# Performance work log

Measured on AMD Instinct MI355X. Metric: run time of the kernel, lower is better.

Reference implementation:

```python
import jax, jax.numpy as jnp
import numpy as np

B_SZ, SEQ = 2, 4096
D_MODEL = 1024
EXPAND = 2
HEADDIM = 64
D_STATE = 128
D_CONV = 4
INTER = EXPAND * D_MODEL            # 2048
NHEADS = INTER // HEADDIM           # 32
CONV_DIM = INTER + 2 * D_STATE      # n_groups = 1
PROJ_DIM = 2 * INTER + 2 * D_STATE + NHEADS
CHUNK = 256
EPS = 1e-5


def setup_inputs() -> dict:
    key = jax.random.key(0)
    k = jax.random.split(key, 6)
    u = jax.random.normal(k[0], (B_SZ, SEQ, D_MODEL), jnp.float32)
    in_proj_w = jax.random.normal(k[1], (D_MODEL, PROJ_DIM), jnp.float32) * 0.02
    conv_w = jax.random.normal(k[2], (CONV_DIM, D_CONV), jnp.float32) * 0.2
    conv_b = jnp.zeros((CONV_DIM,), jnp.float32)
    # dt init in [1e-3, 1e-1], inverse-softplus so softplus(dt_bias) recovers dt
    dt0 = jnp.exp(jax.random.uniform(k[3], (NHEADS,), jnp.float32, np.log(1e-3), np.log(1e-1)))
    dt_bias = jnp.log(jnp.expm1(dt0))
    A_log = jnp.log(jnp.arange(1, NHEADS + 1, dtype=jnp.float32))
    D_param = jnp.ones((NHEADS,), jnp.float32)
    norm_w = jnp.ones((INTER,), jnp.float32)
    out_proj_w = jax.random.normal(k[4], (INTER, D_MODEL), jnp.float32) * 0.02
    return {"u": u, "in_proj_w": in_proj_w, "conv_w": conv_w, "conv_b": conv_b,
            "dt_bias": dt_bias, "A_log": A_log, "D_param": D_param,
            "norm_w": norm_w, "out_proj_w": out_proj_w}


def _silu(x):
    return x * jax.nn.sigmoid(x)


def _causal_conv1d(x, w, b):
    # depthwise causal conv; x (b,s,c), w (c,k); tap k-1 is the current timestep
    k = w.shape[1]
    xp = jnp.pad(x, ((0, 0), (k - 1, 0), (0, 0)))
    y = b
    for i in range(k):
        y = y + xp[:, i:i + x.shape[1], :] * w[:, i]
    return y


def _segsum(x):
    # x (..., l) -> (..., l, l); segsum[i, j] = sum_{j < k <= i} x[k], -inf above diag
    l = x.shape[-1]
    cs = jnp.cumsum(x, -1)
    d = cs[..., :, None] - cs[..., None, :]
    mask = jnp.tril(jnp.ones((l, l), dtype=bool))
    return jnp.where(mask, d, -jnp.inf)


def _ssd(x, dt, A, Bm, Cm):
    # Mamba-2 chunked SSD (ssd_minimal_discrete with X = x*dt, Adt = A*dt).
    # x (b,s,h,p), dt (b,s,h), A (h,), Bm/Cm (b,s,n)
    b, s, h, p = x.shape
    n = Bm.shape[-1]
    c = s // CHUNK
    X = (x * dt[..., None]).reshape(b, c, CHUNK, h, p)          # (b,c,l,h,p)
    Adt = (dt * A).reshape(b, c, CHUNK, h).transpose(0, 3, 1, 2)  # (b,h,c,l)
    Bc = Bm.reshape(b, c, CHUNK, n)
    Cc = Cm.reshape(b, c, CHUNK, n)
    A_cum = jnp.cumsum(Adt, -1)                                  # (b,h,c,l)
    L = jnp.exp(_segsum(Adt))                                    # (b,h,c,l,l) causal decay
    # intra-chunk (diagonal blocks)
    scores = jnp.einsum('bcln,bcsn->bcls', Cc, Bc)               # (b,c,l,l)
    Y_diag = jnp.einsum('bhcls,bcshp->bclhp', scores[:, None] * L, X)
    # per-chunk final states
    decay_states = jnp.exp(A_cum[..., -1:] - A_cum)              # (b,h,c,l)
    states = jnp.einsum('bcln,bhcl,bclhp->bchpn', Bc, decay_states, X)
    # inter-chunk recurrence on chunk states
    A_chunk = jnp.pad(A_cum[..., -1], ((0, 0), (0, 0), (1, 0)))  # (b,h,c+1)
    decay_chunk = jnp.exp(_segsum(A_chunk))                      # (b,h,c+1,c+1)
    states = jnp.concatenate([jnp.zeros_like(states[:, :1]), states], axis=1)  # (b,c+1,h,p,n)
    states = jnp.einsum('bhzc,bchpn->bzhpn', decay_chunk, states)[:, :-1]      # (b,c,h,p,n)
    # state -> output contribution
    Y_off = jnp.einsum('bcln,bchpn,bhcl->bclhp', Cc, states, jnp.exp(A_cum))
    return (Y_diag + Y_off).reshape(b, s, h, p)


def reference(u, in_proj_w, conv_w, conv_b, dt_bias, A_log, D_param, norm_w, out_proj_w):
    b, s, _ = u.shape
    zxbcdt = u @ in_proj_w                                       # (b,s,PROJ_DIM)
    z = zxbcdt[..., :INTER]
    xBC = zxbcdt[..., INTER:INTER + CONV_DIM]
    dt = zxbcdt[..., INTER + CONV_DIM:]
    xBC = _silu(_causal_conv1d(xBC, conv_w, conv_b))
    x = xBC[..., :INTER]
    Bm = xBC[..., INTER:INTER + D_STATE]
    Cm = xBC[..., INTER + D_STATE:]
    dt = jax.nn.softplus(dt + dt_bias)                           # (b,s,h)
    A = -jnp.exp(A_log)                                          # (h,)
    xh = x.reshape(b, s, NHEADS, HEADDIM)
    y = _ssd(xh, dt, A, Bm, Cm) + D_param[None, None, :, None] * xh
    y = y.reshape(b, s, INTER)
    g = y * _silu(z)                                             # gated RMSNorm
    g = g * jax.lax.rsqrt(jnp.mean(g * g, -1, keepdims=True) + EPS) * norm_w
    return g @ out_proj_w
```

## Files before the change

kernel.cpp:

```cpp
#include <hip/hip_runtime.h>
#include <hip/hip_bf16.h>

#define B_SZ 2
#define SEQ 4096
#define DMODEL 1024
#define INTER 2048
#define NHEADS 32
#define HDIM 64
#define DSTATE 128
#define DCONV 4
#define CONVDIM 2304
#define PROJDIM 4384
#define CHUNK 256
#define NCHUNK 16
#define ROWS (B_SZ*SEQ)
#define NGEMM 4352
#define NMAIN 4096

typedef __hip_bfloat16 bf16;
typedef short bfx8 __attribute__((ext_vector_type(8)));
typedef float f32x4 __attribute__((ext_vector_type(4)));

__device__ __forceinline__ float sigmoidf_(float x){ return 1.f/(1.f+expf(-x)); }
__device__ __forceinline__ float b2f(bf16 v){ return __bfloat162float(v); }
__device__ __forceinline__ bf16 f2b(float v){ return __float2bfloat16(v); }
__device__ __forceinline__ float bits2f(unsigned short u){ return __uint_as_float(((unsigned)u) << 16); }
__device__ __forceinline__ unsigned short f2bits(float v){ bf16 t = __float2bfloat16(v); return *(unsigned short*)&t; }

#define MFMA16(a,b,c) __builtin_amdgcn_mfma_f32_16x16x32_bf16(a,b,c,0,0,0)

__global__ void zero_out_kernel(float* o, int n){
  int i = blockIdx.x*256 + threadIdx.x;
  if (i < n) o[i] = 0.f;
}

__global__ __launch_bounds__(256) void transcast_kernel(const float* __restrict__ in,
    bf16* __restrict__ outT, int R, int ld, int coff){
  __shared__ float t[64][65];
  int r0 = blockIdx.y*64, c0 = blockIdx.x*64;
  int tid = threadIdx.x;
  #pragma unroll
  for (int i = 0; i < 16; i++){
    int idx = tid + i*256;
    int r = idx >> 6, c = idx & 63;
    t[r][c] = in[(size_t)(r0+r)*ld + coff + c0 + c];
  }
  __syncthreads();
  #pragma unroll
  for (int i = 0; i < 16; i++){
    int idx = tid + i*256;
    int c = idx >> 6, r = idx & 63;
    outT[(size_t)(c0+c)*R + r0 + r] = f2b(t[r][c]);
  }
}

__device__ __forceinline__ void stage8(const bf16* __restrict__ g, int Kdim,
    int tile0, int k0, char* region, int h, int tid){
  #pragma unroll
  for (int l = 0; l < 2; l++){
    int o  = h*16384 + (l*512 + tid)*16;
    int os = o ^ (((o >> 7) & 7) << 4);
    const bf16* src = g + (size_t)(tile0 + (os >> 7))*Kdim + k0 + ((os & 127) >> 1);
    __builtin_amdgcn_global_load_lds(
      (const __attribute__((address_space(1))) void*)src,
      (__attribute__((address_space(3))) void*)(region + h*16384 + (l*512 + (tid >> 6)*64)*16),
      16, 0, 0);
  }
}
__device__ __forceinline__ bfx8 fr8(const char* region, int row, int colbyte){
  int o = row*128 + colbyte;
  o ^= ((row & 7) << 4);
  return *(const bfx8*)(region + o);
}

#define LGKM0  asm volatile("s_waitcnt lgkmcnt(0)" ::: "memory"); __builtin_amdgcn_sched_barrier(0)
#define VM4    asm volatile("s_waitcnt vmcnt(4)" ::: "memory")
#define VM0    asm volatile("s_waitcnt vmcnt(0)" ::: "memory")
#define BAR    __builtin_amdgcn_s_barrier()
#define PRIO1  __builtin_amdgcn_s_setprio(1)
#define PRIO0  __builtin_amdgcn_s_setprio(0)

#define MFMA_QUAD(MH, NH, BARR)                                                \
  PRIO1;                                                                       \
  _Pragma("unroll") for (int m = 0; m < 4; m++)                                \
    _Pragma("unroll") for (int n = 0; n < 2; n++)                              \
      _Pragma("unroll") for (int kk = 0; kk < 2; kk++)                         \
        acc[(MH)+m][(NH)+n] = MFMA16(aF[m][kk], BARR[n][kk], acc[(MH)+m][(NH)+n]); \
  PRIO0

#define GEMM8_BODY(K_, NBX_)                                                   \
  extern __shared__ char lds[];                                                \
  char* A0 = lds;          char* B0 = lds + 32768;                             \
  char* A1 = lds + 65536;  char* B1 = lds + 98304;                             \
  const int tid = threadIdx.x, lane = tid & 63, wid = tid >> 6;                \
  const int wm = wid >> 2, wn = wid & 3;                                       \
  int nb = (blockIdx.x & 7)*((int)gridDim.x >> 3) + (blockIdx.x >> 3);         \
  const int bx = nb % (NBX_), by = nb / (NBX_);                                \
  const int row0 = by*256, col0 = bx*256;                                      \
  f32x4 acc[8][4] = {};                                                        \
  bfx8 aF[4][2], b01[2][2], b23[2][2];                                         \
  const int frow = lane & 15;                                                  \
  const int fcb0 = (lane >> 4)*16;                                             \
  const int JLAST = (K_)/128 - 1;                                              \
  stage8(Bt, K_, col0, 0,  B0, 0, tid);                                        \
  stage8(Bt, K_, col0, 0,  B0, 1, tid);                                        \
  stage8(A,  K_, row0, 0,  A0, 0, tid);                                        \
  stage8(A,  K_, row0, 0,  A0, 1, tid);                                        \
  stage8(Bt, K_, col0, 64, B1, 0, tid);                                        \
  stage8(Bt, K_, col0, 64, B1, 1, tid);                                        \
  VM4;                                                                         \
  BAR;                                                                         \
  _Pragma("unroll 1")                                                          \
  for (int j = 0; j <= JLAST; j++){                                            \
    const int kO  = j*128 + 64;                                                \
    const int kS1 = (j*128 + 128) & ((K_) - 1);                                \
    const int kS2 = (j*128 + 192) & ((K_) - 1);                                \
    stage8(A, K_, row0, kO, A1, 0, tid);                                       \
    _Pragma("unroll") for (int m = 0; m < 4; m++)                              \
      _Pragma("unroll") for (int kk = 0; kk < 2; kk++)                         \
        aF[m][kk] = fr8(A0, wm*128 + m*16 + frow, kk*64 + fcb0);               \
    _Pragma("unroll") for (int n = 0; n < 2; n++)                              \
      _Pragma("unroll") for (int kk = 0; kk < 2; kk++)                         \
        b01[n][kk] = fr8(B0, wn*64 + n*16 + frow, kk*64 + fcb0);               \
    LGKM0;                                                                     \
    MFMA_QUAD(0, 0, b01);                                                      \
    BAR;                                                                       \
    stage8(A, K_, row0, kO, A1, 1, tid);                                       \
    _Pragma("unroll") for (int n = 0; n < 2; n++)                              \
      _Pragma("unroll") for (int kk = 0; kk < 2; kk++)                         \
        b23[n][kk] = fr8(B0, wn*64 + (n+2)*16 + frow, kk*64 + fcb0);           \
    LGKM0;                                                                     \
    MFMA_QUAD(0, 2, b23);                                                      \
    BAR;                                                                       \
    if (j < JLAST) stage8(Bt, K_, col0, kS1, B0, 0, tid);                      \
    _Pragma("unroll") for (int m = 0; m < 4; m++)                              \
      _Pragma("unroll") for (int kk = 0; kk < 2; kk++)                         \
        aF[m][kk] = fr8(A0, wm*128 + (m+4)*16 + frow, kk*64 + fcb0);           \
    LGKM0;                                                                     \
    MFMA_QUAD(4, 0, b01);                                                      \
    BAR;                                                                       \
    if (j < JLAST){ stage8(Bt, K_, col0, kS1, B0, 1, tid); VM4; }              \
    else { VM0; }                                                              \
    MFMA_QUAD(4, 2, b23);                                                      \
    BAR;                                                                       \
    if (j < JLAST) stage8(A, K_, row0, kS1, A0, 0, tid);                       \
    _Pragma("unroll") for (int m = 0; m < 4; m++)                              \
      _Pragma("unroll") for (int kk = 0; kk < 2; kk++)                         \
        aF[m][kk] = fr8(A1, wm*128 + m*16 + frow, kk*64 + fcb0);               \
    _Pragma("unroll") for (int n = 0; n < 2; n++)                              \
      _Pragma("unroll") for (int kk = 0; kk < 2; kk++)                         \
        b01[n][kk] = fr8(B1, wn*64 + n*16 + frow, kk*64 + fcb0);               \
    LGKM0;                                                                     \
    MFMA_QUAD(0, 0, b01);                                                      \
    BAR;                                                                       \
    if (j < JLAST) stage8(A, K_, row0, kS1, A0, 1, tid);                       \
    _Pragma("unroll") for (int n = 0; n < 2; n++)                              \
      _Pragma("unroll") for (int kk = 0; kk < 2; kk++)                         \
        b23[n][kk] = fr8(B1, wn*64 + (n+2)*16 + frow, kk*64 + fcb0);           \
    LGKM0;                                                                     \
    MFMA_QUAD(0, 2, b23);                                                      \
    BAR;                                                                       \
    if (j < JLAST) stage8(Bt, K_, col0, kS2, B1, 0, tid);                      \
    _Pragma("unroll") for (int m = 0; m < 4; m++)                              \
      _Pragma("unroll") for (int kk = 0; kk < 2; kk++)                         \
        aF[m][kk] = fr8(A1, wm*128 + (m+4)*16 + frow, kk*64 + fcb0);           \
    LGKM0;                                                                     \
    MFMA_QUAD(4, 0, b01);                                                      \
    BAR;                                                                       \
    if (j < JLAST) stage8(Bt, K_, col0, kS2, B1, 1, tid);                      \
    VM4;                                                                       \
    MFMA_QUAD(4, 2, b23);                                                      \
    BAR;                                                                       \
  }

#define SST_STRIDE 280

__global__ __launch_bounds__(512, 2) void gemm8_inproj(const bf16* __restrict__ A,
    const bf16* __restrict__ Bt, bf16* __restrict__ z, bf16* __restrict__ xbc){
  GEMM8_BODY(DMODEL, 16)
  unsigned short* sst = (unsigned short*)lds;
  #pragma unroll 1
  for (int half = 0; half < 2; half++){
    if (wm == half){
      #pragma unroll
      for (int m = 0; m < 8; m++)
        #pragma unroll
        for (int n = 0; n < 4; n++)
          #pragma unroll
          for (int r = 0; r < 4; r++){
            int rl = m*16 + (lane>>4)*4 + r;
            sst[rl*SST_STRIDE + wn*64 + n*16 + (lane&15)] = f2bits(acc[m][n][r]);
          }
    }
    BAR;
    #pragma unroll
    for (int i = 0; i < 8; i++){
      int q = tid + i*512;
      int rl = q >> 5, c8 = (q & 31)*8;
      bfx8 v = *(const bfx8*)(sst + rl*SST_STRIDE + c8);
      int gr = row0 + half*128 + rl, gc = col0 + c8;
      if (gc < INTER) *(bfx8*)(z + (size_t)gr*INTER + gc) = v;
      else            *(bfx8*)(xbc + (size_t)gr*CONVDIM + (gc - INTER)) = v;
    }
    BAR;
  }
}

#define MFMA_GEMM_BODY(K_, EPILOGUE)                                           \
  __shared__ unsigned short As[128*64];                                        \
  __shared__ unsigned short Bs[128*64];                                        \
  const int tid = threadIdx.x;                                                 \
  const int lane = tid & 63, wid = tid >> 6;                                   \
  const int wm = wid >> 1, wn = wid & 1;                                       \
  const int row0 = blockIdx.y*128, col0 = blockIdx.x*128;                      \
  f32x4 acc[4][4] = {};                                                        \
  const int rstg = wid*32 + ((lane>>3)&7);                                     \
  const int kstg = (lane&7)*8;                                                 \
  for (int k0 = 0; k0 < (K_); k0 += 64){                                       \
    _Pragma("unroll")                                                          \
    for (int j = 0; j < 4; j++){                                               \
      const bf16* gA = A + (size_t)(row0 + rstg + j*8)*(K_) + k0 + kstg;       \
      __builtin_amdgcn_global_load_lds(                                        \
        (const __attribute__((address_space(1))) void*)gA,                     \
        (__attribute__((address_space(3))) void*)(As + (wid*32 + j*8)*64),     \
        16, 0, 0);                                                             \
      const bf16* gB = Bt + (size_t)(col0 + rstg + j*8)*(K_) + k0 + kstg;      \
      __builtin_amdgcn_global_load_lds(                                        \
        (const __attribute__((address_space(1))) void*)gB,                     \
        (__attribute__((address_space(3))) void*)(Bs + (wid*32 + j*8)*64),     \
        16, 0, 0);                                                             \
    }                                                                          \
    __syncthreads();                                                           \
    _Pragma("unroll")                                                          \
    for (int kk = 0; kk < 2; kk++){                                            \
      bfx8 af[4], bfr[4];                                                      \
      _Pragma("unroll")                                                        \
      for (int m = 0; m < 4; m++)                                              \
        af[m] = *(const bfx8*)(As + (wm*64 + m*16 + (lane&15))*64              \
                               + kk*32 + (lane>>4)*8);                         \
      _Pragma("unroll")                                                        \
      for (int n = 0; n < 4; n++)                                              \
        bfr[n] = *(const bfx8*)(Bs + (wn*64 + n*16 + (lane&15))*64             \
                                + kk*32 + (lane>>4)*8);                        \
      _Pragma("unroll")                                                        \
      for (int m = 0; m < 4; m++)                                              \
        _Pragma("unroll")                                                      \
        for (int n = 0; n < 4; n++)                                            \
          acc[m][n] = MFMA16(af[m], bfr[n], acc[m][n]);                        \
    }                                                                          \
    __syncthreads();                                                           \
  }                                                                            \
  _Pragma("unroll")                                                            \
  for (int m = 0; m < 4; m++){                                                 \
    int row = row0 + wm*64 + m*16 + (lane>>4)*4;                               \
    _Pragma("unroll")                                                          \
    for (int n = 0; n < 4; n++){                                               \
      int col = col0 + wn*64 + n*16 + (lane&15);                               \
      _Pragma("unroll")                                                        \
      for (int r = 0; r < 4; r++){                                             \
        float v = acc[m][n][r];                                                \
        int rr = row + r;                                                      \
        EPILOGUE                                                               \
      }                                                                        \
    }                                                                          \
  }

__global__ __launch_bounds__(256) void gemm_mfma_inproj(const bf16* __restrict__ A,
    const bf16* __restrict__ Bt, bf16* __restrict__ z, bf16* __restrict__ xbc){
  MFMA_GEMM_BODY(DMODEL,
    if (col < INTER) z[(size_t)rr*INTER + col] = f2b(v);
    else             xbc[(size_t)rr*CONVDIM + (col - INTER)] = f2b(v);
  )
}
__global__ __launch_bounds__(256) void gemm_mfma_strip(const bf16* __restrict__ A,
    const bf16* __restrict__ Bt, bf16* __restrict__ xbc){
  MFMA_GEMM_BODY(DMODEL,
    xbc[(size_t)rr*CONVDIM + 2048 + col] = f2b(v);
  )
}
__global__ __launch_bounds__(256) void gemm_mfma_outproj(const bf16* __restrict__ A,
    const bf16* __restrict__ Bt, float* __restrict__ C){
  MFMA_GEMM_BODY(INTER,
    C[(size_t)rr*DMODEL + col] = v;
  )
}

__global__ __launch_bounds__(256) void dt_partial(const float* __restrict__ u,
    const float* __restrict__ w_in, float* __restrict__ partial,
    unsigned short* __restrict__ u_bf){
  __shared__ float wsm[128][33];
  __shared__ float us[64][133];
  int ks = blockIdx.x, row0 = blockIdx.y*64;
  int k0 = ks*128;
  int tid = threadIdx.x;
  #pragma unroll
  for (int i = 0; i < 16; i++){
    int idx = tid + i*256;
    int r = idx >> 5, c = idx & 31;
    wsm[r][c] = w_in[(size_t)(k0 + r)*PROJDIM + NGEMM + c];
  }
  #pragma unroll
  for (int i = 0; i < 8; i++){
    int idx = tid + i*256;
    int r = idx >> 5, c4 = idx & 31;
    float4 v = *(const float4*)(u + (size_t)(row0 + r)*DMODEL + k0 + c4*4);
    us[r][c4*4+0] = v.x; us[r][c4*4+1] = v.y; us[r][c4*4+2] = v.z; us[r][c4*4+3] = v.w;
    ushort4 w;
    w.x = f2bits(v.x); w.y = f2bits(v.y); w.z = f2bits(v.z); w.w = f2bits(v.w);
    *(ushort4*)(u_bf + (size_t)(row0 + r)*DMODEL + k0 + c4*4) = w;
  }
  __syncthreads();
  int col = tid & 31, r0 = tid >> 5;
  float acc[8] = {};
  #pragma unroll 4
  for (int kk4 = 0; kk4 < 32; kk4++){
    float4 uv[8];
    #pragma unroll
    for (int i = 0; i < 8; i++)
      uv[i] = *(const float4*)&us[r0 + i*8][kk4*4];
    #pragma unroll
    for (int j = 0; j < 4; j++){
      float wv = wsm[kk4*4 + j][col];
      #pragma unroll
      for (int i = 0; i < 8; i++){
        float uvj = (j == 0) ? uv[i].x : (j == 1) ? uv[i].y : (j == 2) ? uv[i].z : uv[i].w;
        acc[i] = fmaf(uvj, wv, acc[i]);
      }
    }
  }
  #pragma unroll
  for (int i = 0; i < 8; i++)
    partial[((size_t)ks*ROWS + row0 + r0 + i*8)*NHEADS + col] = acc[i];
}

__global__ __launch_bounds__(256) void conv_kernel(const bf16* __restrict__ xbc,
    const float* __restrict__ cw, const float* __restrict__ cb,
    bf16* __restrict__ x, bf16* __restrict__ Bm, bf16* __restrict__ Cm){
  int ch = blockIdx.x*256 + threadIdx.x;
  int t0 = blockIdx.y*64;
  int b  = blockIdx.z;
  float w0 = cw[ch*4+0], w1 = cw[ch*4+1], w2 = cw[ch*4+2], w3 = cw[ch*4+3];
  float bia = cb[ch];
  const bf16* src = xbc + (size_t)(b*SEQ)*CONVDIM + ch;
  float xm3 = 0.f, xm2 = 0.f, xm1 = 0.f;
  if (t0 > 0){
    xm3 = b2f(src[(size_t)(t0-3)*CONVDIM]);
    xm2 = b2f(src[(size_t)(t0-2)*CONVDIM]);
    xm1 = b2f(src[(size_t)(t0-1)*CONVDIM]);
  }
  bf16* dst; size_t dstride;
  if (ch < INTER)             { dst = x  + (size_t)(b*SEQ + t0)*INTER  + ch;                 dstride = INTER; }
  else if (ch < INTER+DSTATE) { dst = Bm + (size_t)(b*SEQ + t0)*DSTATE + (ch-INTER);         dstride = DSTATE; }
  else                        { dst = Cm + (size_t)(b*SEQ + t0)*DSTATE + (ch-INTER-DSTATE);  dstride = DSTATE; }
  #pragma unroll 4
  for (int i = 0; i < 64; i++){
    float xc = b2f(src[(size_t)(t0+i)*CONVDIM]);
    float acc = bia;
    acc = fmaf(xm3, w0, acc);
    acc = fmaf(xm2, w1, acc);
    acc = fmaf(xm1, w2, acc);
    acc = fmaf(xc,  w3, acc);
    float v = acc * sigmoidf_(acc);
    dst[(size_t)i*dstride] = f2b(v);
    xm3 = xm2; xm2 = xm1; xm1 = xc;
  }
}

__global__ __launch_bounds__(256) void acum_fused(const float* __restrict__ partial,
    const float* __restrict__ dt_bias, const float* __restrict__ A_log,
    float* __restrict__ dt, float* __restrict__ Acum){
  int bi = blockIdx.x;
  int c = bi & 15; int h = (bi >> 4) & 31; int b = bi >> 9;
  int l = threadIdx.x;
  __shared__ float sbuf[CHUNK];
  int t = c*CHUNK + l;
  size_t idx = (size_t)(b*SEQ + t)*NHEADS + h;
  float s = dt_bias[h];
  #pragma unroll
  for (int ks = 0; ks < 8; ks++)
    s += partial[(size_t)ks*ROWS*NHEADS + idx];
  float v = (s > 20.f) ? s : log1pf(expf(s));
  dt[idx] = v;
  float A = -expf(A_log[h]);
  sbuf[l] = v * A;
  __syncthreads();
  for (int off = 1; off < CHUNK; off <<= 1){
    float add = (l >= off) ? sbuf[l-off] : 0.f;
    __syncthreads();
    sbuf[l] += add;
    __syncthreads();
  }
  Acum[(size_t)bi*CHUNK + l] = sbuf[l];
}

__global__ __launch_bounds__(256) void scores_mfma(const bf16* __restrict__ Bm,
    const bf16* __restrict__ Cm, bf16* __restrict__ S){
  int bc = blockIdx.x;
  int b = bc >> 4, c = bc & 15;
  int tid = threadIdx.x, lane = tid & 63;
  int task = blockIdx.y*4 + (tid >> 6);
  if (task >= 10) return;
  int rb = (task >= 6) ? 3 : (task >= 3) ? 2 : (task >= 1) ? 1 : 0;
  int j = task - rb*(rb+1)/2;
  const bf16* Crow = Cm + (size_t)(b*SEQ + c*CHUNK)*DSTATE;
  const bf16* Brow = Bm + (size_t)(b*SEQ + c*CHUNK)*DSTATE;
  f32x4 acc[4][4] = {};
  #pragma unroll
  for (int kk = 0; kk < 4; kk++){
    bfx8 af[4], bfr[4];
    #pragma unroll
    for (int m = 0; m < 4; m++)
      af[m] = *(const bfx8*)(Crow + (size_t)(rb*64 + m*16 + (lane&15))*DSTATE + kk*32 + (lane>>4)*8);
    #pragma unroll
    for (int n = 0; n < 4; n++)
      bfr[n] = *(const bfx8*)(Brow + (size_t)(j*64 + n*16 + (lane&15))*DSTATE + kk*32 + (lane>>4)*8);
    #pragma unroll
    for (int m = 0; m < 4; m++)
      #pragma unroll
      for (int n = 0; n < 4; n++)
        acc[m][n] = MFMA16(af[m], bfr[n], acc[m][n]);
  }
  bf16* dst = S + (size_t)bc*CHUNK*CHUNK;
  #pragma unroll
  for (int m = 0; m < 4; m++)
    #pragma unroll
    for (int n = 0; n < 4; n++)
      #pragma unroll
      for (int r = 0; r < 4; r++)
        dst[(size_t)(rb*64 + m*16 + (lane>>4)*4 + r)*CHUNK + j*64 + n*16 + (lane&15)]
          = f2b(acc[m][n][r]);
}

__global__ __launch_bounds__(256) void xwt_kernel(const bf16* __restrict__ x,
    const bf16* __restrict__ Bm, const float* __restrict__ dt,
    const float* __restrict__ Acum, bf16* __restrict__ xwt, bf16* __restrict__ bt){
  int pt = blockIdx.x, tt = blockIdx.y, b = blockIdx.z;
  int tid = threadIdx.x;
  __shared__ unsigned short tile[64][72];
  __shared__ float wf[64];
  int t0 = tt*64;
  if (pt < 32){
    int h = pt, c = t0 >> 8;
    if (tid < 64){
      const float* AcB = Acum + ((size_t)(b*NHEADS + h)*NCHUNK + c)*CHUNK;
      int t = t0 + tid;
      wf[tid] = dt[(size_t)(b*SEQ + t)*NHEADS + h] * expf(AcB[255] - AcB[t & 255]);
    }
    __syncthreads();
    const bf16* src = x + (size_t)(b*SEQ + t0)*INTER + pt*64;
    #pragma unroll
    for (int i = 0; i < 2; i++){
      int u = tid + i*256;
      int r = u >> 3, po = (u & 7)*8;
      bfx8 v = *(const bfx8*)(src + (size_t)r*INTER + po);
      float d = wf[r];
      #pragma unroll
      for (int j = 0; j < 8; j++)
        tile[r][po + j] = f2bits(bits2f((unsigned short)v[j]) * d);
    }
    __syncthreads();
    bf16* dst = xwt + ((size_t)(b*INTER) + pt*64)*SEQ + t0;
    #pragma unroll
    for (int i = 0; i < 2; i++){
      int u = tid + i*256;
      int p = u >> 3, tc = (u & 7)*8;
      bfx8 v;
      #pragma unroll
      for (int j = 0; j < 8; j++) v[j] = (short)tile[tc + j][p];
      *(bfx8*)(dst + (size_t)p*SEQ + tc) = v;
    }
  } else {
    int n0 = (pt - 32)*64;
    const bf16* src = Bm + (size_t)(b*SEQ + t0)*DSTATE + n0;
    #pragma unroll
    for (int i = 0; i < 2; i++){
      int u = tid + i*256;
      int r = u >> 3, po = (u & 7)*8;
      bfx8 v = *(const bfx8*)(src + (size_t)r*DSTATE + po);
      *(bfx8*)&tile[r][po] = v;
    }
    __syncthreads();
    bf16* dst = bt + ((size_t)(b*DSTATE) + n0)*SEQ + t0;
    #pragma unroll
    for (int i = 0; i < 2; i++){
      int u = tid + i*256;
      int p = u >> 3, tc = (u & 7)*8;
      bfx8 v;
      #pragma unroll
      for (int j = 0; j < 8; j++) v[j] = (short)tile[tc + j][p];
      *(bfx8*)(dst + (size_t)p*SEQ + tc) = v;
    }
  }
}

__global__ __launch_bounds__(256) void chunk_states_mfma(const bf16* __restrict__ xwt,
    const bf16* __restrict__ bt, float* __restrict__ states){
  int bi = blockIdx.x;
  int h = bi & 31; int c = (bi >> 5) & 15; int b = bi >> 9;
  int tid = threadIdx.x, lane = tid & 63, w = tid >> 6;
  int wm = w >> 1, wn = w & 1;
  const bf16* Arow = xwt + ((size_t)(b*INTER) + h*64)*SEQ + c*CHUNK;
  const bf16* Brow = bt + (size_t)(b*DSTATE)*SEQ + c*CHUNK;
  f32x4 acc[2][4] = {};
  #pragma unroll
  for (int kk = 0; kk < 8; kk++){
    bfx8 af[2], bfr[4];
    #pragma unroll
    for (int m = 0; m < 2; m++)
      af[m] = *(const bfx8*)(Arow + (size_t)(wm*32 + m*16 + (lane&15))*SEQ + kk*32 + (lane>>4)*8);
    #pragma unroll
    for (int n = 0; n < 4; n++)
      bfr[n] = *(const bfx8*)(Brow + (size_t)(wn*64 + n*16 + (lane&15))*SEQ + kk*32 + (lane>>4)*8);
    #pragma unroll
    for (int m = 0; m < 2; m++)
      #pragma unroll
      for (int n = 0; n < 4; n++)
        acc[m][n] = MFMA16(af[m], bfr[n], acc[m][n]);
  }
  float* dst = states + (size_t)bi*HDIM*DSTATE;
  #pragma unroll
  for (int m = 0; m < 2; m++)
    #pragma unroll
    for (int n = 0; n < 4; n++)
      #pragma unroll
      for (int r = 0; r < 4; r++){
        int p = wm*32 + m*16 + (lane>>4)*4 + r;
        int nn = wn*64 + n*16 + (lane&15);
        dst[(size_t)p*DSTATE + nn] = acc[m][n][r];
      }
}

__global__ __launch_bounds__(256) void scan_kernel(float* __restrict__ states,
    const float* __restrict__ Acum){
  int idx = blockIdx.x*256 + threadIdx.x;
  int n = idx & 127; int p = (idx >> 7) & 63; int h = (idx >> 13) & 31; int b = idx >> 18;
  float R = 0.f;
  for (int c = 0; c < NCHUNK; c++){
    size_t o = (((size_t)((b*NCHUNK + c)*NHEADS + h))*HDIM + p)*DSTATE + n;
    float s = states[o];
    states[o] = R;
    float dA = expf(Acum[((size_t)(b*NHEADS + h)*NCHUNK + c)*CHUNK + CHUNK-1]);
    R = R*dA + s;
  }
}

__global__ __launch_bounds__(256, 3) void ydiag_mfma(
    const bf16* x, const float* __restrict__ dt,
    const float* __restrict__ Acum, const bf16* __restrict__ Sg,
    const bf16* __restrict__ Cm, const float* __restrict__ states,
    const float* __restrict__ Dp, bf16* y){
  int bi = blockIdx.x;
  int h = bi & 31; int c = (bi >> 5) & 15; int b = bi >> 9;
  int bc = b*NCHUNK + c;
  int tid = threadIdx.x, lane = tid & 63, w = tid >> 6;

  __shared__ unsigned short XdtT[64*264];
  __shared__ unsigned short pool[128*72];
  __shared__ float Acs[CHUNK];
  __shared__ float dts[CHUNK];

  const float* AcBase = Acum + ((size_t)(b*NHEADS + h)*NCHUNK + c)*CHUNK;
  Acs[tid] = AcBase[tid];
  dts[tid] = dt[(size_t)(b*SEQ + c*CHUNK + tid)*NHEADS + h];
  {
    const float* src = states + (size_t)bi*HDIM*DSTATE;
    #pragma unroll
    for (int i = 0; i < 32; i++){
      int idx = tid + i*256;
      int p = idx >> 7, n = idx & 127;
      pool[p*136 + n] = f2bits(src[idx]);
    }
  }
  __syncthreads();

  const bf16* Crow = Cm + (size_t)(b*SEQ + c*CHUNK)*DSTATE;

  f32x4 accY[4][4] = {};
  #pragma unroll
  for (int kk = 0; kk < 4; kk++){
    bfx8 af[4], bfr[4];
    #pragma unroll
    for (int m = 0; m < 4; m++)
      af[m] = *(const bfx8*)(Crow + (size_t)(w*64 + m*16 + (lane&15))*DSTATE + kk*32 + (lane>>4)*8);
    #pragma unroll
    for (int n = 0; n < 4; n++)
      bfr[n] = *(const bfx8*)(pool + (n*16 + (lane&15))*136 + kk*32 + (lane>>4)*8);
    #pragma unroll
    for (int m = 0; m < 4; m++)
      #pragma unroll
      for (int n = 0; n < 4; n++)
        accY[m][n] = MFMA16(af[m], bfr[n], accY[m][n]);
  }
  {
    float eAl[4][4];
    #pragma unroll
    for (int m = 0; m < 4; m++)
      #pragma unroll
      for (int r = 0; r < 4; r++)
        eAl[m][r] = expf(Acs[w*64 + m*16 + (lane>>4)*4 + r]);
    #pragma unroll
    for (int m = 0; m < 4; m++)
      #pragma unroll
      for (int n = 0; n < 4; n++)
        #pragma unroll
        for (int r = 0; r < 4; r++)
          accY[m][n][r] *= eAl[m][r];
  }
  __syncthreads();

  #pragma unroll 1
  for (int q = 0; q < 2; q++){
    const bf16* xg = x + (size_t)(b*SEQ + c*CHUNK + q*128)*INTER + h*HDIM;
    #pragma unroll
    for (int i = 0; i < 4; i++){
      int u = tid + i*256;
      int s = u >> 3, p0 = (u & 7)*8;
      bfx8 v = *(const bfx8*)(xg + (size_t)s*INTER + p0);
      float d = dts[q*128 + s];
      bfx8 o;
      #pragma unroll
      for (int j = 0; j < 8; j++)
        o[j] = (short)f2bits(bits2f((unsigned short)v[j]) * d);
      *(bfx8*)(pool + s*72 + p0) = o;
    }
    __syncthreads();
    {
      int p = tid & 63, sb = tid >> 6;
      #pragma unroll
      for (int i = 0; i < 4; i++){
        int s0 = (sb + i*4)*8;
        bfx8 v;
        #pragma unroll
        for (int j = 0; j < 8; j++)
          v[j] = (short)pool[(s0 + j)*72 + p];
        *(bfx8*)(XdtT + p*264 + q*128 + s0) = v;
      }
    }
    __syncthreads();
  }

  const bf16* Srow = Sg + (size_t)bc*CHUNK*CHUNK + (size_t)(w*64)*CHUNK;
  float Dh = Dp[h];
  for (int j = 0; j <= w; j++){
    int s0 = j*64;
    bfx8 wfr[4][2];
    if (j < w){
      float m_ = Acs[s0 + 63];
      float rowf[4];
      #pragma unroll
      for (int m = 0; m < 4; m++)
        rowf[m] = expf(Acs[w*64 + m*16 + (lane&15)] - m_);
      #pragma unroll
      for (int kk = 0; kk < 2; kk++){
        float colf[8];
        #pragma unroll
        for (int t = 0; t < 8; t++)
          colf[t] = expf(m_ - Acs[s0 + kk*32 + (lane>>4)*8 + t]);
        #pragma unroll
        for (int m = 0; m < 4; m++){
          bfx8 raw = *(const bfx8*)(Srow + (size_t)(m*16 + (lane&15))*CHUNK + s0 + kk*32 + (lane>>4)*8);
          bfx8 o;
          #pragma unroll
          for (int t = 0; t < 8; t++)
            o[t] = (short)f2bits(bits2f((unsigned short)raw[t]) * rowf[m] * colf[t]);
          wfr[m][kk] = o;
        }
      }
    } else {
      #pragma unroll
      for (int kk = 0; kk < 2; kk++)
        #pragma unroll
        for (int m = 0; m < 4; m++){
          int lg = w*64 + m*16 + (lane&15);
          float Al = Acs[lg];
          bfx8 raw = *(const bfx8*)(Srow + (size_t)(m*16 + (lane&15))*CHUNK + s0 + kk*32 + (lane>>4)*8);
          bfx8 o;
          #pragma unroll
          for (int t = 0; t < 8; t++){
            int sg = s0 + kk*32 + (lane>>4)*8 + t;
            float v;
            if (sg > lg)       v = 0.f;
            else if (sg == lg) v = bits2f((unsigned short)raw[t]) + Dh/dts[lg];
            else               v = bits2f((unsigned short)raw[t]) * expf(Al - Acs[sg]);
            o[t] = (short)f2bits(v);
          }
          wfr[m][kk] = o;
        }
    }
    #pragma unroll
    for (int kk = 0; kk < 2; kk++){
      bfx8 bfr[4];
      #pragma unroll
      for (int n = 0; n < 4; n++)
        bfr[n] = *(const bfx8*)(XdtT + (n*16 + (lane&15))*264 + s0 + kk*32 + (lane>>4)*8);
      #pragma unroll
      for (int m = 0; m < 4; m++)
        #pragma unroll
        for (int n = 0; n < 4; n++)
          accY[m][n] = MFMA16(wfr[m][kk], bfr[n], accY[m][n]);
    }
  }
  bf16* yg = y + (size_t)(b*SEQ + c*CHUNK)*INTER + h*HDIM;
  #pragma unroll
  for (int m = 0; m < 4; m++)
    #pragma unroll
    for (int n = 0; n < 4; n++)
      #pragma unroll
      for (int r = 0; r < 4; r++)
        yg[(size_t)(w*64 + m*16 + (lane>>4)*4 + r)*INTER + n*16 + (lane&15)]
          = f2b(accY[m][n][r]);
}

__global__ __launch_bounds__(256) void gatenorm_kernel(bf16* __restrict__ y,
    const bf16* __restrict__ z, const float* __restrict__ nw){
  int row = blockIdx.x;
  const bf16* zr = z + (size_t)row*INTER;
  bf16* yr = y + (size_t)row*INTER;
  int tid = threadIdx.x;
  bfx8 zv = *(const bfx8*)(zr + tid*8);
  bfx8 yv = *(const bfx8*)(yr + tid*8);
  float g[8]; float ss = 0.f;
  #pragma unroll
  for (int j = 0; j < 8; j++){
    float zf = bits2f((unsigned short)zv[j]);
    float gv = bits2f((unsigned short)yv[j]) * zf * sigmoidf_(zf);
    g[j] = gv; ss += gv*gv;
  }
  #pragma unroll
  for (int off = 32; off > 0; off >>= 1) ss += __shfl_down(ss, off);
  __shared__ float red[4];
  __shared__ float stot;
  int lane = tid & 63, wid = tid >> 6;
  if (lane == 0) red[wid] = ss;
  __syncthreads();
  if (tid == 0) stot = rsqrtf((red[0]+red[1]+red[2]+red[3]) * (1.f/INTER) + 1e-5f);
  __syncthreads();
  float sc = stot;
  float4 nw0 = *(const float4*)(nw + tid*8);
  float4 nw1 = *(const float4*)(nw + tid*8 + 4);
  bfx8 o;
  o[0] = (short)f2bits(g[0]*sc*nw0.x);
  o[1] = (short)f2bits(g[1]*sc*nw0.y);
  o[2] = (short)f2bits(g[2]*sc*nw0.z);
  o[3] = (short)f2bits(g[3]*sc*nw0.w);
  o[4] = (short)f2bits(g[4]*sc*nw1.x);
  o[5] = (short)f2bits(g[5]*sc*nw1.y);
  o[6] = (short)f2bits(g[6]*sc*nw1.z);
  o[7] = (short)f2bits(g[7]*sc*nw1.w);
  *(bfx8*)(yr + tid*8) = o;
}

extern "C" void kernel_launch(void* const* d_in, const int* in_sizes, int n_in,
                              void* d_out, int out_size, void* d_ws, size_t ws_size,
                              hipStream_t stream){
  const float* u    = (const float*)d_in[0];
  const float* w_in = (const float*)d_in[1];
  const float* cw   = (const float*)d_in[2];
  const float* cb   = (const float*)d_in[3];
  const float* dtb  = (const float*)d_in[4];
  const float* Alog = (const float*)d_in[5];
  const float* Dp   = (const float*)d_in[6];
  const float* nw   = (const float*)d_in[7];
  const float* w_out= (const float*)d_in[8];
  float* out = (float*)d_out;
  char* ws = (char*)d_ws;

  const size_t OFF_Z     = 0;
  const size_t OFF_XBC   = 33554432;
  const size_t OFF_DT    = 67108864;
  const size_t OFF_ACUM  = 68157440;
  const size_t OFF_X     = 71303168;
  const size_t OFF_UBF   = 104857600;
  const size_t OFF_WINT  = 121634816;
  const size_t OFF_XWT   = 104857600;
  const size_t OFF_BM    = 138412032;
  const size_t OFF_CM    = 140509184;
  const size_t OFF_BT    = 143654912;
  const size_t OFF_WOUTT = 145752064;
  const size_t OFF_PART  = 149946368;
  const size_t NEED      = 158334976;

  if (ws_size < NEED){
    zero_out_kernel<<<(out_size + 255)/256, 256, 0, stream>>>(out, out_size);
    return;
  }

  bf16*  z      = (bf16*)(ws + OFF_Z);
  bf16*  xbc    = (bf16*)(ws + OFF_XBC);
  float* states = (float*)(ws + OFF_XBC);
  float* dt     = (float*)(ws + OFF_DT);
  float* Acum   = (float*)(ws + OFF_ACUM);
  bf16*  x      = (bf16*)(ws + OFF_X);
  bf16*  y      = (bf16*)(ws + OFF_X);
  bf16*  u_bf   = (bf16*)(ws + OFF_UBF);
  bf16*  w_inT  = (bf16*)(ws + OFF_WINT);
  bf16*  xwt    = (bf16*)(ws + OFF_XWT);
  bf16*  Bm     = (bf16*)(ws + OFF_BM);
  bf16*  Cm     = (bf16*)(ws + OFF_CM);
  bf16*  bt     = (bf16*)(ws + OFF_BT);
  bf16*  w_outT = (bf16*)(ws + OFF_WOUTT);
  float* part   = (float*)(ws + OFF_PART);
  bf16*  S      = (bf16*)(ws + OFF_PART);

  bool use8 = true;
  if (hipFuncSetAttribute((const void*)gemm8_inproj,
        hipFuncAttributeMaxDynamicSharedMemorySize, 131072) != hipSuccess) use8 = false;

  dt_partial<<<dim3(8, ROWS/64), 256, 0, stream>>>(u, w_in, part, (unsigned short*)u_bf);
  transcast_kernel<<<dim3(NGEMM/64, DMODEL/64), 256, 0, stream>>>(w_in, w_inT, DMODEL, PROJDIM, 0);
  if (use8){
    gemm8_inproj<<<512, 512, 131072, stream>>>(u_bf, w_inT, z, xbc);
    gemm_mfma_strip<<<dim3(2, ROWS/128), 256, 0, stream>>>(u_bf, w_inT + (size_t)NMAIN*DMODEL, xbc);
  } else {
    gemm_mfma_inproj<<<dim3(NGEMM/128, ROWS/128), 256, 0, stream>>>(u_bf, w_inT, z, xbc);
  }
  conv_kernel<<<dim3(9, SEQ/64, B_SZ), 256, 0, stream>>>(xbc, cw, cb, x, Bm, Cm);
  acum_fused<<<B_SZ*NHEADS*NCHUNK, 256, 0, stream>>>(part, dtb, Alog, dt, Acum);
  scores_mfma<<<dim3(B_SZ*NCHUNK, 3), 256, 0, stream>>>(Bm, Cm, S);
  xwt_kernel<<<dim3(34, 64, 2), 256, 0, stream>>>(x, Bm, dt, Acum, xwt, bt);
  chunk_states_mfma<<<B_SZ*NCHUNK*NHEADS, 256, 0, stream>>>(xwt, bt, states);
  scan_kernel<<<(B_SZ*NHEADS*HDIM*DSTATE)/256, 256, 0, stream>>>(states, Acum);
  ydiag_mfma<<<B_SZ*NCHUNK*NHEADS, 256, 0, stream>>>(x, dt, Acum, S, Cm, states, Dp, y);
  transcast_kernel<<<dim3(DMODEL/64, INTER/64), 256, 0, stream>>>(w_out, w_outT, INTER, DMODEL, 0);
  gatenorm_kernel<<<ROWS, 256, 0, stream>>>(y, z, nw);
  gemm_mfma_outproj<<<dim3(DMODEL/128, ROWS/128), 256, 0, stream>>>(y, w_outT, out);
}
```

Baseline: 344.9 us.

## Merge independent kernels into combined launches and remap out-proj tiles

Merges pairs of independent kernels into single launches that branch on block index: dt_partial with the w_in transpose-cast, acum with the scores MFMA, and gatenorm with the w_out transpose-cast. This cuts launch count and lets the two pieces of work overlap on the GPU. The out-proj GEMM now uses a 1D grid with a remapped block order to change cache locality. ydiag also loads states as float4 vectors when converting them to bf16. The costs are larger shared-memory footprints per combined kernel and divergent block roles.

Result: slower. 402.8 us (+16.8%).

```diff
diff --git a/kernel.cpp b/kernel.cpp
--- a/kernel.cpp
+++ b/kernel.cpp
@@ -32,26 +32,6 @@
 __global__ void zero_out_kernel(float* o, int n){
   int i = blockIdx.x*256 + threadIdx.x;
   if (i < n) o[i] = 0.f;
-}
-
-__global__ __launch_bounds__(256) void transcast_kernel(const float* __restrict__ in,
-    bf16* __restrict__ outT, int R, int ld, int coff){
-  __shared__ float t[64][65];
-  int r0 = blockIdx.y*64, c0 = blockIdx.x*64;
-  int tid = threadIdx.x;
-  #pragma unroll
-  for (int i = 0; i < 16; i++){
-    int idx = tid + i*256;
-    int r = idx >> 6, c = idx & 63;
-    t[r][c] = in[(size_t)(r0+r)*ld + coff + c0 + c];
-  }
-  __syncthreads();
-  #pragma unroll
-  for (int i = 0; i < 16; i++){
-    int idx = tid + i*256;
-    int c = idx >> 6, r = idx & 63;
-    outT[(size_t)(c0+c)*R + r0 + r] = f2b(t[r][c]);
-  }
 }
 
 __device__ __forceinline__ void stage8(const bf16* __restrict__ g, int Kdim,
@@ -206,13 +186,13 @@
   }
 }
 
-#define MFMA_GEMM_BODY(K_, EPILOGUE)                                           \
+#define MFMA_GEMM_BODY(K_, ROW0_, COL0_, EPILOGUE)                             \
   __shared__ unsigned short As[128*64];                                        \
   __shared__ unsigned short Bs[128*64];                                        \
   const int tid = threadIdx.x;                                                 \
   const int lane = tid & 63, wid = tid >> 6;                                   \
   const int wm = wid >> 1, wn = wid & 1;                                       \
-  const int row0 = blockIdx.y*128, col0 = blockIdx.x*128;                      \
+  const int row0 = (ROW0_), col0 = (COL0_);                                    \
   f32x4 acc[4][4] = {};                                                        \
   const int rstg = wid*32 + ((lane>>3)&7);                                     \
   const int kstg = (lane&7)*8;                                                 \
@@ -267,70 +247,89 @@
 
 __global__ __launch_bounds__(256) void gemm_mfma_inproj(const bf16* __restrict__ A,
     const bf16* __restrict__ Bt, bf16* __restrict__ z, bf16* __restrict__ xbc){
-  MFMA_GEMM_BODY(DMODEL,
+  MFMA_GEMM_BODY(DMODEL, blockIdx.y*128, blockIdx.x*128,
     if (col < INTER) z[(size_t)rr*INTER + col] = f2b(v);
     else             xbc[(size_t)rr*CONVDIM + (col - INTER)] = f2b(v);
   )
 }
 __global__ __launch_bounds__(256) void gemm_mfma_strip(const bf16* __restrict__ A,
     const bf16* __restrict__ Bt, bf16* __restrict__ xbc){
-  MFMA_GEMM_BODY(DMODEL,
+  MFMA_GEMM_BODY(DMODEL, blockIdx.y*128, blockIdx.x*128,
     xbc[(size_t)rr*CONVDIM + 2048 + col] = f2b(v);
   )
 }
 __global__ __launch_bounds__(256) void gemm_mfma_outproj(const bf16* __restrict__ A,
     const bf16* __restrict__ Bt, float* __restrict__ C){
-  MFMA_GEMM_BODY(INTER,
+  int nbo = (blockIdx.x & 7)*64 + (blockIdx.x >> 3);
+  MFMA_GEMM_BODY(INTER, (nbo >> 3)*128, (nbo & 7)*128,
     C[(size_t)rr*DMODEL + col] = v;
   )
 }
 
-__global__ __launch_bounds__(256) void dt_partial(const float* __restrict__ u,
+__global__ __launch_bounds__(256) void prep_kernel(const float* __restrict__ u,
     const float* __restrict__ w_in, float* __restrict__ partial,
-    unsigned short* __restrict__ u_bf){
-  __shared__ float wsm[128][33];
-  __shared__ float us[64][133];
-  int ks = blockIdx.x, row0 = blockIdx.y*64;
-  int k0 = ks*128;
-  int tid = threadIdx.x;
-  #pragma unroll
-  for (int i = 0; i < 16; i++){
-    int idx = tid + i*256;
-    int r = idx >> 5, c = idx & 31;
-    wsm[r][c] = w_in[(size_t)(k0 + r)*PROJDIM + NGEMM + c];
-  }
-  #pragma unroll
-  for (int i = 0; i < 8; i++){
-    int idx = tid + i*256;
-    int r = idx >> 5, c4 = idx & 31;
-    float4 v = *(const float4*)(u + (size_t)(row0 + r)*DMODEL + k0 + c4*4);
-    us[r][c4*4+0] = v.x; us[r][c4*4+1] = v.y; us[r][c4*4+2] = v.z; us[r][c4*4+3] = v.w;
-    ushort4 w;
-    w.x = f2bits(v.x); w.y = f2bits(v.y); w.z = f2bits(v.z); w.w = f2bits(v.w);
-    *(ushort4*)(u_bf + (size_t)(row0 + r)*DMODEL + k0 + c4*4) = w;
-  }
-  __syncthreads();
-  int col = tid & 31, r0 = tid >> 5;
-  float acc[8] = {};
-  #pragma unroll 4
-  for (int kk4 = 0; kk4 < 32; kk4++){
-    float4 uv[8];
+    unsigned short* __restrict__ u_bf, bf16* __restrict__ w_inT){
+  __shared__ char smem[50944];
+  int blk = blockIdx.x, tid = threadIdx.x;
+  if (blk < 1024){
+    float (*wsm)[33]  = (float(*)[33])smem;
+    float (*us)[133]  = (float(*)[133])(smem + 16896);
+    int ks = blk & 7, row0 = (blk >> 3)*64;
+    int k0 = ks*128;
+    #pragma unroll
+    for (int i = 0; i < 16; i++){
+      int idx = tid + i*256;
+      wsm[idx >> 5][idx & 31] = w_in[(size_t)(k0 + (idx >> 5))*PROJDIM + NGEMM + (idx & 31)];
+    }
+    #pragma unroll
+    for (int i = 0; i < 8; i++){
+      int idx = tid + i*256;
+      int r = idx >> 5, c4 = idx & 31;
+      float4 v = *(const float4*)(u + (size_t)(row0 + r)*DMODEL + k0 + c4*4);
+      us[r][c4*4+0] = v.x; us[r][c4*4+1] = v.y; us[r][c4*4+2] = v.z; us[r][c4*4+3] = v.w;
+      ushort4 w;
+      w.x = f2bits(v.x); w.y = f2bits(v.y); w.z = f2bits(v.z); w.w = f2bits(v.w);
+      *(ushort4*)(u_bf + (size_t)(row0 + r)*DMODEL + k0 + c4*4) = w;
+    }
+    __syncthreads();
+    int col = tid & 31, r0 = tid >> 5;
+    float acc[8] = {};
+    #pragma unroll 4
+    for (int kk4 = 0; kk4 < 32; kk4++){
+      float4 uv[8];
+      #pragma unroll
+      for (int i = 0; i < 8; i++)
+        uv[i] = *(const float4*)&us[r0 + i*8][kk4*4];
+      #pragma unroll
+      for (int j = 0; j < 4; j++){
+        float wv = wsm[kk4*4 + j][col];
+        #pragma unroll
+        for (int i = 0; i < 8; i++){
+          float uvj = (j == 0) ? uv[i].x : (j == 1) ? uv[i].y : (j == 2) ? uv[i].z : uv[i].w;
+          acc[i] = fmaf(uvj, wv, acc[i]);
+        }
+      }
+    }
     #pragma unroll
     for (int i = 0; i < 8; i++)
-      uv[i] = *(const float4*)&us[r0 + i*8][kk4*4];
-    #pragma unroll
-    for (int j = 0; j < 4; j++){
-      float wv = wsm[kk4*4 + j][col];
-      #pragma unroll
-      for (int i = 0; i < 8; i++){
-        float uvj = (j == 0) ? uv[i].x : (j == 1) ? uv[i].y : (j == 2) ? uv[i].z : uv[i].w;
-        acc[i] = fmaf(uvj, wv, acc[i]);
-      }
-    }
-  }
-  #pragma unroll
-  for (int i = 0; i < 8; i++)
-    partial[((size_t)ks*ROWS + row0 + r0 + i*8)*NHEADS + col] = acc[i];
+      partial[((size_t)ks*ROWS + row0 + r0 + i*8)*NHEADS + col] = acc[i];
+  } else {
+    float (*t)[65] = (float(*)[65])smem;
+    int idx = blk - 1024;
+    int c0 = (idx % 68)*64, r0 = (idx / 68)*64;
+    #pragma unroll
+    for (int i = 0; i < 16; i++){
+      int q = tid + i*256;
+      t[q >> 6][q & 63] = w_in[(size_t)(r0 + (q >> 6))*PROJDIM + c0 + (q & 63)];
+    }
+    __syncthreads();
+    #pragma unroll
+    for (int i = 0; i < 16; i++){
+      int q = tid + i*256;
+      int c = q >> 6, r = q & 63;
+      w_inT[(size_t)(c0 + c)*DMODEL + r0 + r] = f2b(t[r][c]);
+    }
+  }
 }
 
 __global__ __launch_bounds__(256) void conv_kernel(const bf16* __restrict__ xbc,
@@ -366,69 +365,71 @@
   }
 }
 
-__global__ __launch_bounds__(256) void acum_fused(const float* __restrict__ partial,
+__global__ __launch_bounds__(256) void acum_scores(const float* __restrict__ partial,
     const float* __restrict__ dt_bias, const float* __restrict__ A_log,
-    float* __restrict__ dt, float* __restrict__ Acum){
-  int bi = blockIdx.x;
-  int c = bi & 15; int h = (bi >> 4) & 31; int b = bi >> 9;
-  int l = threadIdx.x;
+    float* __restrict__ dt, float* __restrict__ Acum,
+    const bf16* __restrict__ Bm, const bf16* __restrict__ Cm, bf16* __restrict__ S){
   __shared__ float sbuf[CHUNK];
-  int t = c*CHUNK + l;
-  size_t idx = (size_t)(b*SEQ + t)*NHEADS + h;
-  float s = dt_bias[h];
-  #pragma unroll
-  for (int ks = 0; ks < 8; ks++)
-    s += partial[(size_t)ks*ROWS*NHEADS + idx];
-  float v = (s > 20.f) ? s : log1pf(expf(s));
-  dt[idx] = v;
-  float A = -expf(A_log[h]);
-  sbuf[l] = v * A;
-  __syncthreads();
-  for (int off = 1; off < CHUNK; off <<= 1){
-    float add = (l >= off) ? sbuf[l-off] : 0.f;
-    __syncthreads();
-    sbuf[l] += add;
-    __syncthreads();
-  }
-  Acum[(size_t)bi*CHUNK + l] = sbuf[l];
-}
-
-__global__ __launch_bounds__(256) void scores_mfma(const bf16* __restrict__ Bm,
-    const bf16* __restrict__ Cm, bf16* __restrict__ S){
-  int bc = blockIdx.x;
-  int b = bc >> 4, c = bc & 15;
-  int tid = threadIdx.x, lane = tid & 63;
-  int task = blockIdx.y*4 + (tid >> 6);
-  if (task >= 10) return;
-  int rb = (task >= 6) ? 3 : (task >= 3) ? 2 : (task >= 1) ? 1 : 0;
-  int j = task - rb*(rb+1)/2;
-  const bf16* Crow = Cm + (size_t)(b*SEQ + c*CHUNK)*DSTATE;
-  const bf16* Brow = Bm + (size_t)(b*SEQ + c*CHUNK)*DSTATE;
-  f32x4 acc[4][4] = {};
-  #pragma unroll
-  for (int kk = 0; kk < 4; kk++){
-    bfx8 af[4], bfr[4];
+  int blk = blockIdx.x, tid = threadIdx.x;
+  if (blk < 1024){
+    int bi = blk;
+    int c = bi & 15; int h = (bi >> 4) & 31; int b = bi >> 9;
+    int l = tid;
+    int t = c*CHUNK + l;
+    size_t idx = (size_t)(b*SEQ + t)*NHEADS + h;
+    float s = dt_bias[h];
+    #pragma unroll
+    for (int ks = 0; ks < 8; ks++)
+      s += partial[(size_t)ks*ROWS*NHEADS + idx];
+    float v = (s > 20.f) ? s : log1pf(expf(s));
+    dt[idx] = v;
+    float A = -expf(A_log[h]);
+    sbuf[l] = v * A;
+    __syncthreads();
+    for (int off = 1; off < CHUNK; off <<= 1){
+      float add = (l >= off) ? sbuf[l-off] : 0.f;
+      __syncthreads();
+      sbuf[l] += add;
+      __syncthreads();
+    }
+    Acum[(size_t)bi*CHUNK + l] = sbuf[l];
+  } else {
+    int sb = blk - 1024;
+    int bc = sb & 31;
+    int b = bc >> 4, c = bc & 15;
+    int lane = tid & 63;
+    int task = (sb >> 5)*4 + (tid >> 6);
+    if (task >= 10) return;
+    int rb = (task >= 6) ? 3 : (task >= 3) ? 2 : (task >= 1) ? 1 : 0;
+    int j = task - rb*(rb+1)/2;
+    const bf16* Crow = Cm + (size_t)(b*SEQ + c*CHUNK)*DSTATE;
+    const bf16* Brow = Bm + (size_t)(b*SEQ + c*CHUNK)*DSTATE;
+    f32x4 acc[4][4] = {};
+    #pragma unroll
+    for (int kk = 0; kk < 4; kk++){
+      bfx8 af[4], bfr[4];
+      #pragma unroll
+      for (int m = 0; m < 4; m++)
+        af[m] = *(const bfx8*)(Crow + (size_t)(rb*64 + m*16 + (lane&15))*DSTATE + kk*32 + (lane>>4)*8);
+      #pragma unroll
+      for (int n = 0; n < 4; n++)
+        bfr[n] = *(const bfx8*)(Brow + (size_t)(j*64 + n*16 + (lane&15))*DSTATE + kk*32 + (lane>>4)*8);
+      #pragma unroll
+      for (int m = 0; m < 4; m++)
+        #pragma unroll
+        for (int n = 0; n < 4; n++)
+          acc[m][n] = MFMA16(af[m], bfr[n], acc[m][n]);
+    }
+    bf16* dst = S + (size_t)bc*CHUNK*CHUNK;
     #pragma unroll
     for (int m = 0; m < 4; m++)
-      af[m] = *(const bfx8*)(Crow + (size_t)(rb*64 + m*16 + (lane&15))*DSTATE + kk*32 + (lane>>4)*8);
-    #pragma unroll
-    for (int n = 0; n < 4; n++)
-      bfr[n] = *(const bfx8*)(Brow + (size_t)(j*64 + n*16 + (lane&15))*DSTATE + kk*32 + (lane>>4)*8);
-    #pragma unroll
-    for (int m = 0; m < 4; m++)
       #pragma unroll
       for (int n = 0; n < 4; n++)
-        acc[m][n] = MFMA16(af[m], bfr[n], acc[m][n]);
-  }
-  bf16* dst = S + (size_t)bc*CHUNK*CHUNK;
-  #pragma unroll
-  for (int m = 0; m < 4; m++)
-    #pragma unroll
-    for (int n = 0; n < 4; n++)
-      #pragma unroll
-      for (int r = 0; r < 4; r++)
-        dst[(size_t)(rb*64 + m*16 + (lane>>4)*4 + r)*CHUNK + j*64 + n*16 + (lane&15)]
-          = f2b(acc[m][n][r]);
+        #pragma unroll
+        for (int r = 0; r < 4; r++)
+          dst[(size_t)(rb*64 + m*16 + (lane>>4)*4 + r)*CHUNK + j*64 + n*16 + (lane&15)]
+            = f2b(acc[m][n][r]);
+  }
 }
 
 __global__ __launch_bounds__(256) void xwt_kernel(const bf16* __restrict__ x,
@@ -565,10 +566,13 @@
   {
     const float* src = states + (size_t)bi*HDIM*DSTATE;
     #pragma unroll
-    for (int i = 0; i < 32; i++){
-      int idx = tid + i*256;
-      int p = idx >> 7, n = idx & 127;
-      pool[p*136 + n] = f2bits(src[idx]);
+    for (int i = 0; i < 8; i++){
+      int q = tid + i*256;
+      float4 v = ((const float4*)src)[q];
+      int p = q >> 5, n = (q & 31)*4;
+      ushort4 o;
+      o.x = f2bits(v.x); o.y = f2bits(v.y); o.z = f2bits(v.z); o.w = f2bits(v.w);
+      *(ushort4*)(pool + p*136 + n) = o;
     }
   }
   __syncthreads();
@@ -711,43 +715,61 @@
           = f2b(accY[m][n][r]);
 }
 
-__global__ __launch_bounds__(256) void gatenorm_kernel(bf16* __restrict__ y,
-    const bf16* __restrict__ z, const float* __restrict__ nw){
-  int row = blockIdx.x;
-  const bf16* zr = z + (size_t)row*INTER;
-  bf16* yr = y + (size_t)row*INTER;
-  int tid = threadIdx.x;
-  bfx8 zv = *(const bfx8*)(zr + tid*8);
-  bfx8 yv = *(const bfx8*)(yr + tid*8);
-  float g[8]; float ss = 0.f;
-  #pragma unroll
-  for (int j = 0; j < 8; j++){
-    float zf = bits2f((unsigned short)zv[j]);
-    float gv = bits2f((unsigned short)yv[j]) * zf * sigmoidf_(zf);
-    g[j] = gv; ss += gv*gv;
-  }
-  #pragma unroll
-  for (int off = 32; off > 0; off >>= 1) ss += __shfl_down(ss, off);
+__global__ __launch_bounds__(256) void gate_wout(bf16* __restrict__ y,
+    const bf16* __restrict__ z, const float* __restrict__ nw,
+    const float* __restrict__ w_out, bf16* __restrict__ w_outT){
+  __shared__ float t[64][65];
   __shared__ float red[4];
   __shared__ float stot;
-  int lane = tid & 63, wid = tid >> 6;
-  if (lane == 0) red[wid] = ss;
-  __syncthreads();
-  if (tid == 0) stot = rsqrtf((red[0]+red[1]+red[2]+red[3]) * (1.f/INTER) + 1e-5f);
-  __syncthreads();
-  float sc = stot;
-  float4 nw0 = *(const float4*)(nw + tid*8);
-  float4 nw1 = *(const float4*)(nw + tid*8 + 4);
-  bfx8 o;
-  o[0] = (short)f2bits(g[0]*sc*nw0.x);
-  o[1] = (short)f2bits(g[1]*sc*nw0.y);
-  o[2] = (short)f2bits(g[2]*sc*nw0.z);
-  o[3] = (short)f2bits(g[3]*sc*nw0.w);
-  o[4] = (short)f2bits(g[4]*sc*nw1.x);
-  o[5] = (short)f2bits(g[5]*sc*nw1.y);
-  o[6] = (short)f2bits(g[6]*sc*nw1.z);
-  o[7] = (short)f2bits(g[7]*sc*nw1.w);
-  *(bfx8*)(yr + tid*8) = o;
+  int blk = blockIdx.x, tid = threadIdx.x;
+  if (blk < ROWS){
+    const bf16* zr = z + (size_t)blk*INTER;
+    bf16* yr = y + (size_t)blk*INTER;
+    bfx8 zv = *(const bfx8*)(zr + tid*8);
+    bfx8 yv = *(const bfx8*)(yr + tid*8);
+    float g[8]; float ss = 0.f;
+    #pragma unroll
+    for (int j = 0; j < 8; j++){
+      float zf = bits2f((unsigned short)zv[j]);
+      float gv = bits2f((unsigned short)yv[j]) * zf * sigmoidf_(zf);
+      g[j] = gv; ss += gv*gv;
+    }
+    #pragma unroll
+    for (int off = 32; off > 0; off >>= 1) ss += __shfl_down(ss, off);
+    int lane = tid & 63, wid = tid >> 6;
+    if (lane == 0) red[wid] = ss;
+    __syncthreads();
+    if (tid == 0) stot = rsqrtf((red[0]+red[1]+red[2]+red[3]) * (1.f/INTER) + 1e-5f);
+    __syncthreads();
+    float sc = stot;
+    float4 nw0 = *(const float4*)(nw + tid*8);
+    float4 nw1 = *(const float4*)(nw + tid*8 + 4);
+    bfx8 o;
+    o[0] = (short)f2bits(g[0]*sc*nw0.x);
+    o[1] = (short)f2bits(g[1]*sc*nw0.y);
+    o[2] = (short)f2bits(g[2]*sc*nw0.z);
+    o[3] = (short)f2bits(g[3]*sc*nw0.w);
+    o[4] = (short)f2bits(g[4]*sc*nw1.x);
+    o[5] = (short)f2bits(g[5]*sc*nw1.y);
+    o[6] = (short)f2bits(g[6]*sc*nw1.z);
+    o[7] = (short)f2bits(g[7]*sc*nw1.w);
+    *(bfx8*)(yr + tid*8) = o;
+  } else {
+    int idx = blk - ROWS;
+    int c0 = (idx & 15)*64, r0 = (idx >> 4)*64;
+    #pragma unroll
+    for (int i = 0; i < 16; i++){
+      int q = tid + i*256;
+      t[q >> 6][q & 63] = w_out[(size_t)(r0 + (q >> 6))*DMODEL + c0 + (q & 63)];
+    }
+    __syncthreads();
+    #pragma unroll
+    for (int i = 0; i < 16; i++){
+      int q = tid + i*256;
+      int c = q >> 6, r = q & 63;
+      w_outT[(size_t)(c0 + c)*INTER + r0 + r] = f2b(t[r][c]);
+    }
+  }
 }
 
 extern "C" void kernel_launch(void* const* d_in, const int* in_sizes, int n_in,
@@ -806,8 +828,7 @@
   if (hipFuncSetAttribute((const void*)gemm8_inproj,
         hipFuncAttributeMaxDynamicSharedMemorySize, 131072) != hipSuccess) use8 = false;
 
-  dt_partial<<<dim3(8, ROWS/64), 256, 0, stream>>>(u, w_in, part, (unsigned short*)u_bf);
-  transcast_kernel<<<dim3(NGEMM/64, DMODEL/64), 256, 0, stream>>>(w_in, w_inT, DMODEL, PROJDIM, 0);
+  prep_kernel<<<2112, 256, 0, stream>>>(u, w_in, part, (unsigned short*)u_bf, w_inT);
   if (use8){
     gemm8_inproj<<<512, 512, 131072, stream>>>(u_bf, w_inT, z, xbc);
     gemm_mfma_strip<<<dim3(2, ROWS/128), 256, 0, stream>>>(u_bf, w_inT + (size_t)NMAIN*DMODEL, xbc);
@@ -815,13 +836,11 @@
     gemm_mfma_inproj<<<dim3(NGEMM/128, ROWS/128), 256, 0, stream>>>(u_bf, w_inT, z, xbc);
   }
   conv_kernel<<<dim3(9, SEQ/64, B_SZ), 256, 0, stream>>>(xbc, cw, cb, x, Bm, Cm);
-  acum_fused<<<B_SZ*NHEADS*NCHUNK, 256, 0, stream>>>(part, dtb, Alog, dt, Acum);
-  scores_mfma<<<dim3(B_SZ*NCHUNK, 3), 256, 0, stream>>>(Bm, Cm, S);
+  acum_scores<<<1120, 256, 0, stream>>>(part, dtb, Alog, dt, Acum, Bm, Cm, S);
   xwt_kernel<<<dim3(34, 64, 2), 256, 0, stream>>>(x, Bm, dt, Acum, xwt, bt);
   chunk_states_mfma<<<B_SZ*NCHUNK*NHEADS, 256, 0, stream>>>(xwt, bt, states);
   scan_kernel<<<(B_SZ*NHEADS*HDIM*DSTATE)/256, 256, 0, stream>>>(states, Acum);
   ydiag_mfma<<<B_SZ*NCHUNK*NHEADS, 256, 0, stream>>>(x, dt, Acum, S, Cm, states, Dp, y);
-  transcast_kernel<<<dim3(DMODEL/64, INTER/64), 256, 0, stream>>>(w_out, w_outT, INTER, DMODEL, 0);
-  gatenorm_kernel<<<ROWS, 256, 0, stream>>>(y, z, nw);
-  gemm_mfma_outproj<<<dim3(DMODEL/128, ROWS/128), 256, 0, stream>>>(y, w_outT, out);
-}
+  gate_wout<<<ROWS + 512, 256, 0, stream>>>(y, z, nw, w_out, w_outT);
+  gemm_mfma_outproj<<<512, 256, 0, stream>>>(y, w_outT, out);
+}
```
